# Optimization experiments

Hardware: AMD Instinct MI355X
Metric: run time of the kernel (lower is better)

## Reference

```python
import jax, jax.numpy as jnp
import numpy as np
from jax import lax

B, T, D = 8, 4096, 512
UNITS = 512
WINDOW = 2


def setup_inputs() -> dict:
    key = jax.random.key(0)
    k1, k2, k3 = jax.random.split(key, 3)
    x = jax.random.normal(k1, (B, T, D), dtype=jnp.float32)
    # keras kernel shape is (window, 1, input_dim, 3*units); drop the dummy height dim
    kernel = jax.random.uniform(k2, (WINDOW, D, 3 * UNITS), dtype=jnp.float32,
                                minval=-0.05, maxval=0.05)
    bias = jnp.zeros((3 * UNITS,), dtype=jnp.float32)
    return {"x": x, "kernel": kernel, "bias": bias}


def reference(x, kernel, bias):
    window, d_in, u3 = kernel.shape
    units = u3 // 3
    # causal padding: window-1 zeros on the left of the time axis
    xp = jnp.pad(x, ((0, 0), (window - 1, 0), (0, 0)))
    # 1D valid conv -> gates [B, T, 3*units]
    gates = lax.conv_general_dilated(
        xp, kernel, window_strides=(1,), padding='VALID',
        dimension_numbers=('NWC', 'WIO', 'NWC')) + bias
    z = jnp.tanh(gates[..., :units])
    f = jax.nn.sigmoid(gates[..., units:2 * units])
    o = jax.nn.sigmoid(gates[..., 2 * units:])

    # fo-pool recurrence: c_t = f_t * c_{t-1} + (1 - f_t) * z_t ; out_t = o_t * c_t
    def step(c, zfo):
        z_t, f_t, o_t = zfo
        c = f_t * c + (1.0 - f_t) * z_t
        return c, o_t * c

    c0 = jnp.zeros((x.shape[0], units), dtype=x.dtype)
    zT = jnp.swapaxes(z, 0, 1)  # [T, B, U]
    fT = jnp.swapaxes(f, 0, 1)
    oT = jnp.swapaxes(o, 0, 1)
    _, ysT = lax.scan(step, c0, (zT, fT, oT))
    return jnp.swapaxes(ysT, 0, 1)  # [B, T, U] (return_sequences=True)
```

## Files before the change

### kernel.cpp

```cpp
#include <hip/hip_runtime.h>
#include <cstdint>
#include <cstddef>

#define BB   8
#define TT   4096
#define DD   512
#define UU   512
#define NN   1536
#define KK   1024
#define MM   32768
#define NCH  256
#define CHL  16

using bf16x8 = __attribute__((ext_vector_type(8))) __bf16;
using f32x4  = __attribute__((ext_vector_type(4))) float;

__device__ __forceinline__ unsigned short f2bf(float f) {
    unsigned u = __float_as_uint(f);
    u += 0x7fffu + ((u >> 16) & 1u);
    return (unsigned short)(u >> 16);
}
__device__ __forceinline__ float bf2f(unsigned short s) {
    return __uint_as_float(((unsigned)s) << 16);
}
__device__ __forceinline__ float sigf(float x) { return 1.0f / (1.0f + __expf(-x)); }
__device__ __forceinline__ float tanh_(float x) { return 1.0f - 2.0f / (1.0f + __expf(2.0f * x)); }

__device__ __forceinline__ void async16(const void* g, void* l) {
    __builtin_amdgcn_global_load_lds(
        (__attribute__((address_space(1))) void*)g,
        (__attribute__((address_space(3))) void*)l, 16, 0, 0);
}

__global__ void k_prep(const float* __restrict__ x, unsigned short* __restrict__ xpad,
                       const float* __restrict__ kern, unsigned short* __restrict__ kT) {
    int bx = blockIdx.x;
    int by = blockIdx.y;
    int tid = threadIdx.x;
    if (bx < 2049) {
        int q = bx * 256 + tid;
        if (q >= 4097 * 128) return;
        int tp = q >> 7;
        int d  = (q & 127) << 2;
        size_t oi = ((size_t)by * 4097 + tp) * 512 + d;
        ushort4 o;
        if (tp == 0) {
            o.x = o.y = o.z = o.w = 0;
        } else {
            float4 v = *(const float4*)(x + ((size_t)by * 4096 + (tp - 1)) * 512 + d);
            o.x = f2bf(v.x); o.y = f2bf(v.y); o.z = f2bf(v.z); o.w = f2bf(v.w);
        }
        *(ushort4*)(xpad + oi) = o;
    } else {
        __shared__ float tile[32][33];
        int idx = (bx - 2049) * 8 + by;
        int c  = tid & 31;
        int r0 = tid >> 5;
        for (int t8 = 0; t8 < 8; ++t8) {
            int tnum = idx * 8 + t8;
            int k0 = (tnum & 31) * 32;
            int n0 = (tnum >> 5) * 32;
#pragma unroll
            for (int rr = r0; rr < 32; rr += 8)
                tile[rr][c] = kern[(size_t)(k0 + rr) * NN + n0 + c];
            __syncthreads();
#pragma unroll
            for (int rr = r0; rr < 32; rr += 8)
                kT[(size_t)(n0 + rr) * KK + k0 + c] = f2bf(tile[c][rr]);
            __syncthreads();
        }
    }
}


#define STAGE_A(BUF, KT, KH) do { \
    async16(xpad + abase + (size_t)rowS0 * 512 + ((KT) * 64 + (KH) * 32 + kcS0), \
            smem + (BUF) * 65536 + (KH) * 16384 + offL0); \
    async16(xpad + abase + (size_t)rowS1 * 512 + ((KT) * 64 + (KH) * 32 + kcS1), \
            smem + (BUF) * 65536 + (KH) * 16384 + offL1); \
} while (0)

#define STAGE_B(BUF, KT, KH) do { \
    async16(kTg + (size_t)(n0 + rowS0) * 1024 + ((KT) * 64 + (KH) * 32 + kcS0), \
            smem + (BUF) * 65536 + 32768 + (KH) * 16384 + offL0); \
    async16(kTg + (size_t)(n0 + rowS1) * 1024 + ((KT) * 64 + (KH) * 32 + kcS1), \
            smem + (BUF) * 65536 + 32768 + (KH) * 16384 + offL1); \
} while (0)

#define VM4 asm volatile("s_waitcnt vmcnt(4)" ::: "memory")
#define VM2 asm volatile("s_waitcnt vmcnt(2)" ::: "memory")
#define VM0 asm volatile("s_waitcnt vmcnt(0)" ::: "memory")

#define LDS_A(BUF, KS, MR) (*(const bf16x8*)(smem + (BUF) * 65536 + (KS) * 16384 + (MR) * 1024 + ldsA))
#define LDS_B(BUF, KS, NR) (*(const bf16x8*)(smem + (BUF) * 65536 + (KS) * 16384 + (NR) * 1024 + ldsB))

#define PH(DO_R, RBUF, RKS, RMH, AFN, LBN, BFN, AFC, BFC, MH, STG, VMW) \
    __builtin_amdgcn_s_barrier(); \
    if (DO_R) { \
        AFN[0] = LDS_A(RBUF, RKS, (RMH) * 4 + 0); \
        AFN[1] = LDS_A(RBUF, RKS, (RMH) * 4 + 1); \
        AFN[2] = LDS_A(RBUF, RKS, (RMH) * 4 + 2); \
        AFN[3] = LDS_A(RBUF, RKS, (RMH) * 4 + 3); \
        if (LBN) { \
            BFN[0] = LDS_B(RBUF, RKS, 0); \
            BFN[1] = LDS_B(RBUF, RKS, 1); \
            BFN[2] = LDS_B(RBUF, RKS, 2); \
            BFN[3] = LDS_B(RBUF, RKS, 3); \
        } \
    } \
    STG; \
    __builtin_amdgcn_sched_barrier(0); \
    __builtin_amdgcn_s_setprio(1); \
    acc[(MH)*4+0][0] = __builtin_amdgcn_mfma_f32_16x16x32_bf16(AFC[0], BFC[0], acc[(MH)*4+0][0], 0, 0, 0); \
    acc[(MH)*4+0][1] = __builtin_amdgcn_mfma_f32_16x16x32_bf16(AFC[0], BFC[1], acc[(MH)*4+0][1], 0, 0, 0); \
    acc[(MH)*4+0][2] = __builtin_amdgcn_mfma_f32_16x16x32_bf16(AFC[0], BFC[2], acc[(MH)*4+0][2], 0, 0, 0); \
    acc[(MH)*4+0][3] = __builtin_amdgcn_mfma_f32_16x16x32_bf16(AFC[0], BFC[3], acc[(MH)*4+0][3], 0, 0, 0); \
    acc[(MH)*4+1][0] = __builtin_amdgcn_mfma_f32_16x16x32_bf16(AFC[1], BFC[0], acc[(MH)*4+1][0], 0, 0, 0); \
    acc[(MH)*4+1][1] = __builtin_amdgcn_mfma_f32_16x16x32_bf16(AFC[1], BFC[1], acc[(MH)*4+1][1], 0, 0, 0); \
    acc[(MH)*4+1][2] = __builtin_amdgcn_mfma_f32_16x16x32_bf16(AFC[1], BFC[2], acc[(MH)*4+1][2], 0, 0, 0); \
    acc[(MH)*4+1][3] = __builtin_amdgcn_mfma_f32_16x16x32_bf16(AFC[1], BFC[3], acc[(MH)*4+1][3], 0, 0, 0); \
    acc[(MH)*4+2][0] = __builtin_amdgcn_mfma_f32_16x16x32_bf16(AFC[2], BFC[0], acc[(MH)*4+2][0], 0, 0, 0); \
    acc[(MH)*4+2][1] = __builtin_amdgcn_mfma_f32_16x16x32_bf16(AFC[2], BFC[1], acc[(MH)*4+2][1], 0, 0, 0); \
    acc[(MH)*4+2][2] = __builtin_amdgcn_mfma_f32_16x16x32_bf16(AFC[2], BFC[2], acc[(MH)*4+2][2], 0, 0, 0); \
    acc[(MH)*4+2][3] = __builtin_amdgcn_mfma_f32_16x16x32_bf16(AFC[2], BFC[3], acc[(MH)*4+2][3], 0, 0, 0); \
    acc[(MH)*4+3][0] = __builtin_amdgcn_mfma_f32_16x16x32_bf16(AFC[3], BFC[0], acc[(MH)*4+3][0], 0, 0, 0); \
    acc[(MH)*4+3][1] = __builtin_amdgcn_mfma_f32_16x16x32_bf16(AFC[3], BFC[1], acc[(MH)*4+3][1], 0, 0, 0); \
    acc[(MH)*4+3][2] = __builtin_amdgcn_mfma_f32_16x16x32_bf16(AFC[3], BFC[2], acc[(MH)*4+3][2], 0, 0, 0); \
    acc[(MH)*4+3][3] = __builtin_amdgcn_mfma_f32_16x16x32_bf16(AFC[3], BFC[3], acc[(MH)*4+3][3], 0, 0, 0); \
    __builtin_amdgcn_s_setprio(0); \
    VMW;

__global__ __launch_bounds__(512, 2) void k_gemm(
    const unsigned short* __restrict__ xpad,
    const unsigned short* __restrict__ kTg,
    const float* __restrict__ bias,
    unsigned short* __restrict__ gates)
{
    __shared__ char smem[131072];

    const int tid  = threadIdx.x;
    const int wid  = tid >> 6;
    const int lane = tid & 63;
    const int wr   = wid >> 2;
    const int wc   = wid & 3;
    const int lrow = lane & 15;
    const int quad = lane >> 4;

    const int bid = blockIdx.x;
    const int wg  = (bid & 7) * 96 + (bid >> 3);
    const int mt  = wg / 6;
    const int nt  = wg % 6;
    const int m0  = mt * 256;
    const int n0  = nt * 256;
    const int boff = m0 >> 12;
    const size_t abase = (size_t)(m0 + boff) * 512;

    const int off0 = (wid * 2 + 0) * 1024 + lane * 16;
    const int off1 = (wid * 2 + 1) * 1024 + lane * 16;
    const int ln0 = off0 >> 7, ln1 = off1 >> 7;
    const int g80 = ((off0 >> 4) & 7) ^ (ln0 & 7);
    const int g81 = ((off1 >> 4) & 7) ^ (ln1 & 7);
    const int offL0 = off0, offL1 = off1;
    const int rowS0 = ln0 * 2 + (g80 >> 2), rowS1 = ln1 * 2 + (g81 >> 2);
    const int kcS0 = (g80 & 3) * 8,         kcS1 = (g81 & 3) * 8;

    const int lh  = lrow >> 1;
    const int g8f = ((lrow & 1) * 4 + quad) ^ lh;
    const int ldsA = (wr * 64 + lh) * 128 + g8f * 16;
    const int ldsB = 32768 + (wc * 32 + lh) * 128 + g8f * 16;

    f32x4 acc[8][4] = {};
    bf16x8 afS0[4], afS1[4], bfS0[4], bfS1[4];

    STAGE_A(0, 0, 0); STAGE_B(0, 0, 0); STAGE_A(0, 0, 1); STAGE_B(0, 0, 1);
    VM4;
    __builtin_amdgcn_s_barrier();
    afS0[0] = LDS_A(0, 0, 0); afS0[1] = LDS_A(0, 0, 1);
    afS0[2] = LDS_A(0, 0, 2); afS0[3] = LDS_A(0, 0, 3);
    bfS0[0] = LDS_B(0, 0, 0); bfS0[1] = LDS_B(0, 0, 1);
    bfS0[2] = LDS_B(0, 0, 2); bfS0[3] = LDS_B(0, 0, 3);

    for (int i = 0; i < 7; ++i) {
        const int t1 = 2 * i + 1;
        const int t2 = 2 * i + 2;
        PH(1, 0, 0, 1, afS1, 0, bfS0, afS0, bfS0, 0, STAGE_A(1, t1, 0), VM2)
        PH(1, 0, 1, 0, afS0, 1, bfS1, afS1, bfS0, 1, STAGE_B(1, t1, 0), (void)0)
        PH(1, 0, 1, 1, afS1, 0, bfS0, afS0, bfS1, 0, STAGE_A(1, t1, 1), VM2)
        PH(1, 1, 0, 0, afS0, 1, bfS0, afS1, bfS1, 1, STAGE_B(1, t1, 1), (void)0)
        PH(1, 1, 0, 1, afS1, 0, bfS0, afS0, bfS0, 0, STAGE_A(0, t2, 0), VM2)
        PH(1, 1, 1, 0, afS0, 1, bfS1, afS1, bfS0, 1, STAGE_B(0, t2, 0), (void)0)
        PH(1, 1, 1, 1, afS1, 0, bfS0, afS0, bfS1, 0, STAGE_A(0, t2, 1), VM2)
        PH(1, 0, 0, 0, afS0, 1, bfS0, afS1, bfS1, 1, STAGE_B(0, t2, 1), (void)0)
    }
    {
        PH(1, 0, 0, 1, afS1, 0, bfS0, afS0, bfS0, 0, STAGE_A(1, 15, 0), VM2)
        PH(1, 0, 1, 0, afS0, 1, bfS1, afS1, bfS0, 1, STAGE_B(1, 15, 0), (void)0)
        PH(1, 0, 1, 1, afS1, 0, bfS0, afS0, bfS1, 0, STAGE_A(1, 15, 1), VM2)
        PH(1, 1, 0, 0, afS0, 1, bfS0, afS1, bfS1, 1, STAGE_B(1, 15, 1), (void)0)
        PH(1, 1, 0, 1, afS1, 0, bfS0, afS0, bfS0, 0, (void)0,           VM0)
        PH(1, 1, 1, 0, afS0, 1, bfS1, afS1, bfS0, 1, (void)0,           (void)0)
        PH(1, 1, 1, 1, afS1, 0, bfS0, afS0, bfS1, 0, (void)0,           (void)0)
        PH(0, 0, 0, 0, afS0, 0, bfS0, afS1, bfS1, 1, (void)0,           (void)0)
    }

    __syncthreads();
#pragma unroll
    for (int n = 0; n < 4; ++n) {
        int coll = wc * 64 + n * 16 + lrow;
        float bv = bias[n0 + coll];
        int g    = coll >> 3;
        int cb   = (coll & 7) * 2;
#pragma unroll
        for (int m = 0; m < 8; ++m) {
            int rbase = wr * 128 + m * 16 + quad * 4;
#pragma unroll
            for (int r = 0; r < 4; ++r) {
                int row = rbase + r;
                *(unsigned short*)(smem + row * 512 + ((g ^ (row & 7)) * 16) + cb)
                    = f2bf(acc[m][n][r] + bv);
            }
        }
    }
    __syncthreads();
    {
        unsigned short* gbase = gates + (size_t)m0 * NN + n0;
#pragma unroll
        for (int it = 0; it < 16; ++it) {
            int idx = it * 512 + tid;
            int row = idx >> 5;
            int g   = idx & 31;
            bf16x8 v = *(const bf16x8*)(smem + row * 512 + ((g ^ (row & 7)) * 16));
            *(bf16x8*)(gbase + (size_t)row * NN + g * 8) = v;
        }
    }
}

__global__ __launch_bounds__(128) void k_scanA(const unsigned short* __restrict__ gates,
                        float* __restrict__ Fp, float* __restrict__ Ce) {
    const int chunk = blockIdx.x;
    const int b     = blockIdx.y;
    const int u     = threadIdx.x << 2;
    const size_t g0 = ((size_t)b * TT + (size_t)chunk * CHL) * NN + u;

    float c0 = 0, c1 = 0, c2 = 0, c3 = 0;
    float F0 = 1, F1 = 1, F2 = 1, F3 = 1;

    ushort4 bz[8], bf_[8];
#pragma unroll
    for (int j = 0; j < 8; ++j) {
        bz[j]  = *(const ushort4*)(gates + g0 + (size_t)j * NN);
        bf_[j] = *(const ushort4*)(gates + g0 + (size_t)j * NN + UU);
    }
#pragma unroll
    for (int h = 0; h < 2; ++h) {
        ushort4 nz[8], nf[8];
        if (h == 0) {
#pragma unroll
            for (int j = 0; j < 8; ++j) {
                nz[j] = *(const ushort4*)(gates + g0 + (size_t)(8 + j) * NN);
                nf[j] = *(const ushort4*)(gates + g0 + (size_t)(8 + j) * NN + UU);
            }
        }
#pragma unroll
        for (int j = 0; j < 8; ++j) {
            float f0 = sigf(bf2f(bf_[j].x)), z0 = tanh_(bf2f(bz[j].x));
            float f1 = sigf(bf2f(bf_[j].y)), z1 = tanh_(bf2f(bz[j].y));
            float f2 = sigf(bf2f(bf_[j].z)), z2 = tanh_(bf2f(bz[j].z));
            float f3 = sigf(bf2f(bf_[j].w)), z3 = tanh_(bf2f(bz[j].w));
            c0 = f0 * c0 + (1.0f - f0) * z0; F0 *= f0;
            c1 = f1 * c1 + (1.0f - f1) * z1; F1 *= f1;
            c2 = f2 * c2 + (1.0f - f2) * z2; F2 *= f2;
            c3 = f3 * c3 + (1.0f - f3) * z3; F3 *= f3;
        }
        if (h == 0) {
#pragma unroll
            for (int j = 0; j < 8; ++j) { bz[j] = nz[j]; bf_[j] = nf[j]; }
        }
    }
    size_t ci = ((size_t)b * NCH + chunk) * UU + u;
    *(float4*)(Fp + ci) = make_float4(F0, F1, F2, F3);
    *(float4*)(Ce + ci) = make_float4(c0, c1, c2, c3);
}

__global__ __launch_bounds__(128) void k_scanB(const float* __restrict__ Fp,
                        const float* __restrict__ Ce, float* __restrict__ Cin) {
    int gid = blockIdx.x * 128 + threadIdx.x;
    int bb = gid >> 9;
    int uu = gid & 511;
    size_t base = (size_t)bb * NCH * UU + uu;
    float c = 0.0f;
    for (int k0 = 0; k0 < NCH; k0 += 8) {
        float F[8], E[8];
#pragma unroll
        for (int j = 0; j < 8; ++j) {
            F[j] = Fp[base + (size_t)(k0 + j) * UU];
            E[j] = Ce[base + (size_t)(k0 + j) * UU];
        }
#pragma unroll
        for (int j = 0; j < 8; ++j) {
            Cin[base + (size_t)(k0 + j) * UU] = c;
            c = F[j] * c + E[j];
        }
    }
}

__global__ __launch_bounds__(128) void k_scanC(const unsigned short* __restrict__ gates,
                        const float* __restrict__ Cin, float* __restrict__ out) {
    const int chunk = blockIdx.x;
    const int b     = blockIdx.y;
    const int u     = threadIdx.x << 2;
    const size_t g0 = ((size_t)b * TT + (size_t)chunk * CHL) * NN + u;
    size_t o = ((size_t)b * TT + (size_t)chunk * CHL) * UU + u;

    size_t ci = ((size_t)b * NCH + chunk) * UU + u;
    float4 cv = *(const float4*)(Cin + ci);
    float c0 = cv.x, c1 = cv.y, c2 = cv.z, c3 = cv.w;

    ushort4 bz[4], bf_[4], bo[4];
#pragma unroll
    for (int j = 0; j < 4; ++j) {
        bz[j]  = *(const ushort4*)(gates + g0 + (size_t)j * NN);
        bf_[j] = *(const ushort4*)(gates + g0 + (size_t)j * NN + UU);
        bo[j]  = *(const ushort4*)(gates + g0 + (size_t)j * NN + 2 * UU);
    }
#pragma unroll
    for (int k = 0; k < 4; ++k) {
        ushort4 nz[4], nf[4], no[4];
        if (k < 3) {
#pragma unroll
            for (int j = 0; j < 4; ++j) {
                size_t gg = g0 + (size_t)((k + 1) * 4 + j) * NN;
                nz[j] = *(const ushort4*)(gates + gg);
                nf[j] = *(const ushort4*)(gates + gg + UU);
                no[j] = *(const ushort4*)(gates + gg + 2 * UU);
            }
        }
#pragma unroll
        for (int j = 0; j < 4; ++j) {
            float f0 = sigf(bf2f(bf_[j].x)), z0 = tanh_(bf2f(bz[j].x)), o0 = sigf(bf2f(bo[j].x));
            float f1 = sigf(bf2f(bf_[j].y)), z1 = tanh_(bf2f(bz[j].y)), o1 = sigf(bf2f(bo[j].y));
            float f2 = sigf(bf2f(bf_[j].z)), z2 = tanh_(bf2f(bz[j].z)), o2 = sigf(bf2f(bo[j].z));
            float f3 = sigf(bf2f(bf_[j].w)), z3 = tanh_(bf2f(bz[j].w)), o3 = sigf(bf2f(bo[j].w));
            c0 = f0 * c0 + (1.0f - f0) * z0;
            c1 = f1 * c1 + (1.0f - f1) * z1;
            c2 = f2 * c2 + (1.0f - f2) * z2;
            c3 = f3 * c3 + (1.0f - f3) * z3;
            f32x4 ov = { o0 * c0, o1 * c1, o2 * c2, o3 * c3 };
            __builtin_nontemporal_store(ov, (f32x4*)(out + o));
            o += UU;
        }
        if (k < 3) {
#pragma unroll
            for (int j = 0; j < 4; ++j) { bz[j] = nz[j]; bf_[j] = nf[j]; bo[j] = no[j]; }
        }
    }
}

extern "C" void kernel_launch(void* const* d_in, const int* in_sizes, int n_in,
                              void* d_out, int out_size, void* d_ws, size_t ws_size,
                              hipStream_t stream) {
    const float* x    = (const float*)d_in[0];
    const float* kern = (const float*)d_in[1];
    const float* bias = (const float*)d_in[2];
    float* out = (float*)d_out;
    char* ws = (char*)d_ws;

    unsigned short* xpad  = (unsigned short*)(ws + 0);
    unsigned short* kT    = (unsigned short*)(ws + 33562624);
    unsigned short* gates = (unsigned short*)(ws + 36708352);
    float* Fp  = (float*)(ws + 137371648);
    float* Ce  = (float*)(ws + 141565952);
    float* Cin = (float*)(ws + 145760256);

    hipLaunchKernelGGL(k_prep,  dim3(2049 + 24, 8), dim3(256), 0, stream, x, xpad, kern, kT);
    hipLaunchKernelGGL(k_gemm,  dim3(768),          dim3(512), 0, stream, xpad, kT, bias, gates);
    hipLaunchKernelGGL(k_scanA, dim3(NCH, BB),      dim3(128), 0, stream, gates, Fp, Ce);
    hipLaunchKernelGGL(k_scanB, dim3(32),           dim3(128), 0, stream, Fp, Ce, Cin);
    hipLaunchKernelGGL(k_scanC, dim3(NCH, BB),      dim3(128), 0, stream, gates, Cin, out);
}
```

Measured before the change: 309.8 us.

## Fuse three-pass chunked scan into single decoupled-lookback scan kernel

```diff
diff --git a/kernel.cpp b/kernel.cpp
--- a/kernel.cpp
+++ b/kernel.cpp
@@ -9,8 +9,8 @@
 #define NN   1536
 #define KK   1024
 #define MM   32768
-#define NCH  256
-#define CHL  16
+#define NCH2 128
+#define CHL2 32
 
 using bf16x8 = __attribute__((ext_vector_type(8))) __bf16;
 using f32x4  = __attribute__((ext_vector_type(4))) float;
@@ -23,8 +23,12 @@
 __device__ __forceinline__ float bf2f(unsigned short s) {
     return __uint_as_float(((unsigned)s) << 16);
 }
-__device__ __forceinline__ float sigf(float x) { return 1.0f / (1.0f + __expf(-x)); }
-__device__ __forceinline__ float tanh_(float x) { return 1.0f - 2.0f / (1.0f + __expf(2.0f * x)); }
+__device__ __forceinline__ float sigf(float x) {
+    return __builtin_amdgcn_rcpf(1.0f + __expf(-x));
+}
+__device__ __forceinline__ float tanh_(float x) {
+    return 1.0f - 2.0f * __builtin_amdgcn_rcpf(1.0f + __expf(2.0f * x));
+}
 
 __device__ __forceinline__ void async16(const void* g, void* l) {
     __builtin_amdgcn_global_load_lds(
@@ -235,123 +239,162 @@
     }
 }
 
-__global__ __launch_bounds__(128) void k_scanA(const unsigned short* __restrict__ gates,
-                        float* __restrict__ Fp, float* __restrict__ Ce) {
-    const int chunk = blockIdx.x;
-    const int b     = blockIdx.y;
-    const int u     = threadIdx.x << 2;
-    const size_t g0 = ((size_t)b * TT + (size_t)chunk * CHL) * NN + u;
-
-    float c0 = 0, c1 = 0, c2 = 0, c3 = 0;
-    float F0 = 1, F1 = 1, F2 = 1, F3 = 1;
-
-    ushort4 bz[8], bf_[8];
-#pragma unroll
-    for (int j = 0; j < 8; ++j) {
-        bz[j]  = *(const ushort4*)(gates + g0 + (size_t)j * NN);
-        bf_[j] = *(const ushort4*)(gates + g0 + (size_t)j * NN + UU);
-    }
-#pragma unroll
-    for (int h = 0; h < 2; ++h) {
-        ushort4 nz[8], nf[8];
-        if (h == 0) {
-#pragma unroll
-            for (int j = 0; j < 8; ++j) {
-                nz[j] = *(const ushort4*)(gates + g0 + (size_t)(8 + j) * NN);
-                nf[j] = *(const ushort4*)(gates + g0 + (size_t)(8 + j) * NN + UU);
-            }
-        }
-#pragma unroll
-        for (int j = 0; j < 8; ++j) {
-            float f0 = sigf(bf2f(bf_[j].x)), z0 = tanh_(bf2f(bz[j].x));
-            float f1 = sigf(bf2f(bf_[j].y)), z1 = tanh_(bf2f(bz[j].y));
-            float f2 = sigf(bf2f(bf_[j].z)), z2 = tanh_(bf2f(bz[j].z));
-            float f3 = sigf(bf2f(bf_[j].w)), z3 = tanh_(bf2f(bz[j].w));
-            c0 = f0 * c0 + (1.0f - f0) * z0; F0 *= f0;
-            c1 = f1 * c1 + (1.0f - f1) * z1; F1 *= f1;
-            c2 = f2 * c2 + (1.0f - f2) * z2; F2 *= f2;
-            c3 = f3 * c3 + (1.0f - f3) * z3; F3 *= f3;
-        }
-        if (h == 0) {
-#pragma unroll
-            for (int j = 0; j < 8; ++j) { bz[j] = nz[j]; bf_[j] = nf[j]; }
-        }
-    }
-    size_t ci = ((size_t)b * NCH + chunk) * UU + u;
-    *(float4*)(Fp + ci) = make_float4(F0, F1, F2, F3);
-    *(float4*)(Ce + ci) = make_float4(c0, c1, c2, c3);
-}
-
-__global__ __launch_bounds__(128) void k_scanB(const float* __restrict__ Fp,
-                        const float* __restrict__ Ce, float* __restrict__ Cin) {
-    int gid = blockIdx.x * 128 + threadIdx.x;
-    int bb = gid >> 9;
-    int uu = gid & 511;
-    size_t base = (size_t)bb * NCH * UU + uu;
-    float c = 0.0f;
-    for (int k0 = 0; k0 < NCH; k0 += 8) {
-        float F[8], E[8];
-#pragma unroll
-        for (int j = 0; j < 8; ++j) {
-            F[j] = Fp[base + (size_t)(k0 + j) * UU];
-            E[j] = Ce[base + (size_t)(k0 + j) * UU];
-        }
-#pragma unroll
-        for (int j = 0; j < 8; ++j) {
-            Cin[base + (size_t)(k0 + j) * UU] = c;
-            c = F[j] * c + E[j];
-        }
-    }
-}
-
-__global__ __launch_bounds__(128) void k_scanC(const unsigned short* __restrict__ gates,
-                        const float* __restrict__ Cin, float* __restrict__ out) {
-    const int chunk = blockIdx.x;
-    const int b     = blockIdx.y;
-    const int u     = threadIdx.x << 2;
-    const size_t g0 = ((size_t)b * TT + (size_t)chunk * CHL) * NN + u;
-    size_t o = ((size_t)b * TT + (size_t)chunk * CHL) * UU + u;
-
-    size_t ci = ((size_t)b * NCH + chunk) * UU + u;
-    float4 cv = *(const float4*)(Cin + ci);
-    float c0 = cv.x, c1 = cv.y, c2 = cv.z, c3 = cv.w;
-
-    ushort4 bz[4], bf_[4], bo[4];
-#pragma unroll
-    for (int j = 0; j < 4; ++j) {
-        bz[j]  = *(const ushort4*)(gates + g0 + (size_t)j * NN);
-        bf_[j] = *(const ushort4*)(gates + g0 + (size_t)j * NN + UU);
-        bo[j]  = *(const ushort4*)(gates + g0 + (size_t)j * NN + 2 * UU);
-    }
-#pragma unroll
-    for (int k = 0; k < 4; ++k) {
-        ushort4 nz[4], nf[4], no[4];
-        if (k < 3) {
+__global__ __launch_bounds__(128, 4) void k_scan(
+    const unsigned short* __restrict__ gates,
+    float* AggF, float* AggE, float* Inc, unsigned* status,
+    float* __restrict__ out)
+{
+    const int bid   = blockIdx.x;
+    const int chunk = bid & (NCH2 - 1);
+    const int b     = bid >> 7;
+    const int tid   = threadIdx.x;
+    const int u     = tid << 2;
+    const size_t g0 = ((size_t)b * TT + (size_t)chunk * CHL2) * NN + u;
+    const size_t ai = ((size_t)b * NCH2 + chunk) * UU + u;
+    const int    si = b * NCH2 + chunk;
+
+    float c[4]  = {0.f, 0.f, 0.f, 0.f};
+    float Fa[4] = {1.f, 1.f, 1.f, 1.f};
+    {
+        ushort4 bz[4], bf4[4];
+#pragma unroll
+        for (int j = 0; j < 4; ++j) {
+            bz[j]  = *(const ushort4*)(gates + g0 + (size_t)j * NN);
+            bf4[j] = *(const ushort4*)(gates + g0 + (size_t)j * NN + UU);
+        }
+        for (int h = 0; h < 8; ++h) {
+            ushort4 nz[4], nf[4];
+            if (h < 7) {
+#pragma unroll
+                for (int j = 0; j < 4; ++j) {
+                    size_t gg = g0 + (size_t)((h + 1) * 4 + j) * NN;
+                    nz[j] = *(const ushort4*)(gates + gg);
+                    nf[j] = *(const ushort4*)(gates + gg + UU);
+                }
+            }
 #pragma unroll
             for (int j = 0; j < 4; ++j) {
-                size_t gg = g0 + (size_t)((k + 1) * 4 + j) * NN;
-                nz[j] = *(const ushort4*)(gates + gg);
-                nf[j] = *(const ushort4*)(gates + gg + UU);
-                no[j] = *(const ushort4*)(gates + gg + 2 * UU);
-            }
-        }
+                float f0 = sigf(bf2f(bf4[j].x)), z0 = tanh_(bf2f(bz[j].x));
+                float f1 = sigf(bf2f(bf4[j].y)), z1 = tanh_(bf2f(bz[j].y));
+                float f2 = sigf(bf2f(bf4[j].z)), z2 = tanh_(bf2f(bz[j].z));
+                float f3 = sigf(bf2f(bf4[j].w)), z3 = tanh_(bf2f(bz[j].w));
+                c[0] = f0 * c[0] + (1.0f - f0) * z0; Fa[0] *= f0;
+                c[1] = f1 * c[1] + (1.0f - f1) * z1; Fa[1] *= f1;
+                c[2] = f2 * c[2] + (1.0f - f2) * z2; Fa[2] *= f2;
+                c[3] = f3 * c[3] + (1.0f - f3) * z3; Fa[3] *= f3;
+            }
+            if (h < 7) {
+#pragma unroll
+                for (int j = 0; j < 4; ++j) { bz[j] = nz[j]; bf4[j] = nf[j]; }
+            }
+        }
+    }
+#pragma unroll
+    for (int e = 0; e < 4; ++e) {
+        __hip_atomic_store(AggF + ai + e, Fa[e], __ATOMIC_RELAXED, __HIP_MEMORY_SCOPE_AGENT);
+        __hip_atomic_store(AggE + ai + e, c[e],  __ATOMIC_RELAXED, __HIP_MEMORY_SCOPE_AGENT);
+    }
+    __threadfence();
+    __syncthreads();
+    if (tid == 0)
+        __hip_atomic_store(status + si, 1u, __ATOMIC_RELEASE, __HIP_MEMORY_SCOPE_AGENT);
+
+    float carry[4] = {0.f, 0.f, 0.f, 0.f};
+    if (chunk > 0) {
+        float runF[4] = {1.f, 1.f, 1.f, 1.f};
+        int k = chunk - 1;
+        for (;;) {
+            if (k < 0) break;
+            int nb = (k >= 3) ? 4 : (k + 1);
+            unsigned st[4];
+            float Fv[4][4], Ev[4][4], Iv[4][4];
+#pragma unroll
+            for (int j = 0; j < 4; ++j) {
+                if (j < nb)
+                    st[j] = __hip_atomic_load(status + b * NCH2 + (k - j),
+                                              __ATOMIC_ACQUIRE, __HIP_MEMORY_SCOPE_AGENT);
+            }
+#pragma unroll
+            for (int j = 0; j < 4; ++j) {
+                if (j < nb) {
+                    size_t aj = ((size_t)b * NCH2 + (k - j)) * UU + u;
+#pragma unroll
+                    for (int e = 0; e < 4; ++e) {
+                        Fv[j][e] = __hip_atomic_load(AggF + aj + e, __ATOMIC_RELAXED, __HIP_MEMORY_SCOPE_AGENT);
+                        Ev[j][e] = __hip_atomic_load(AggE + aj + e, __ATOMIC_RELAXED, __HIP_MEMORY_SCOPE_AGENT);
+                        Iv[j][e] = __hip_atomic_load(Inc  + aj + e, __ATOMIC_RELAXED, __HIP_MEMORY_SCOPE_AGENT);
+                    }
+                }
+            }
+            bool done = false;
+            int adv = nb;
+            for (int j = 0; j < nb; ++j) {
+                if (st[j] == 0u) { adv = j; break; }
+                if (st[j] == 2u) {
+#pragma unroll
+                    for (int e = 0; e < 4; ++e) carry[e] = fmaf(runF[e], Iv[j][e], carry[e]);
+                    done = true; break;
+                }
+#pragma unroll
+                for (int e = 0; e < 4; ++e) {
+                    carry[e] = fmaf(runF[e], Ev[j][e], carry[e]);
+                    runF[e] *= Fv[j][e];
+                }
+            }
+            if (done) break;
+            k -= adv;
+            if (adv == 0) __builtin_amdgcn_s_sleep(2);
+        }
+    }
+#pragma unroll
+    for (int e = 0; e < 4; ++e) {
+        float inc = fmaf(Fa[e], carry[e], c[e]);
+        __hip_atomic_store(Inc + ai + e, inc, __ATOMIC_RELAXED, __HIP_MEMORY_SCOPE_AGENT);
+    }
+    __threadfence();
+    __syncthreads();
+    if (tid == 0)
+        __hip_atomic_store(status + si, 2u, __ATOMIC_RELEASE, __HIP_MEMORY_SCOPE_AGENT);
+
+    {
+        float c0 = carry[0], c1 = carry[1], c2 = carry[2], c3 = carry[3];
+        size_t o = ((size_t)b * TT + (size_t)chunk * CHL2) * UU + u;
+        ushort4 bz[4], bf4[4], bo[4];
 #pragma unroll
         for (int j = 0; j < 4; ++j) {
-            float f0 = sigf(bf2f(bf_[j].x)), z0 = tanh_(bf2f(bz[j].x)), o0 = sigf(bf2f(bo[j].x));
-            float f1 = sigf(bf2f(bf_[j].y)), z1 = tanh_(bf2f(bz[j].y)), o1 = sigf(bf2f(bo[j].y));
-            float f2 = sigf(bf2f(bf_[j].z)), z2 = tanh_(bf2f(bz[j].z)), o2 = sigf(bf2f(bo[j].z));
-            float f3 = sigf(bf2f(bf_[j].w)), z3 = tanh_(bf2f(bz[j].w)), o3 = sigf(bf2f(bo[j].w));
-            c0 = f0 * c0 + (1.0f - f0) * z0;
-            c1 = f1 * c1 + (1.0f - f1) * z1;
-            c2 = f2 * c2 + (1.0f - f2) * z2;
-            c3 = f3 * c3 + (1.0f - f3) * z3;
-            f32x4 ov = { o0 * c0, o1 * c1, o2 * c2, o3 * c3 };
-            __builtin_nontemporal_store(ov, (f32x4*)(out + o));
-            o += UU;
-        }
-        if (k < 3) {
-#pragma unroll
-            for (int j = 0; j < 4; ++j) { bz[j] = nz[j]; bf_[j] = nf[j]; bo[j] = no[j]; }
+            bz[j]  = *(const ushort4*)(gates + g0 + (size_t)j * NN);
+            bf4[j] = *(const ushort4*)(gates + g0 + (size_t)j * NN + UU);
+            bo[j]  = *(const ushort4*)(gates + g0 + (size_t)j * NN + 2 * UU);
+        }
+        for (int h = 0; h < 8; ++h) {
+            ushort4 nz[4], nf[4], no[4];
+            if (h < 7) {
+#pragma unroll
+                for (int j = 0; j < 4; ++j) {
+                    size_t gg = g0 + (size_t)((h + 1) * 4 + j) * NN;
+                    nz[j] = *(const ushort4*)(gates + gg);
+                    nf[j] = *(const ushort4*)(gates + gg + UU);
+                    no[j] = *(const ushort4*)(gates + gg + 2 * UU);
+                }
+            }
+#pragma unroll
+            for (int j = 0; j < 4; ++j) {
+                float f0 = sigf(bf2f(bf4[j].x)), z0 = tanh_(bf2f(bz[j].x)), o0 = sigf(bf2f(bo[j].x));
+                float f1 = sigf(bf2f(bf4[j].y)), z1 = tanh_(bf2f(bz[j].y)), o1 = sigf(bf2f(bo[j].y));
+                float f2 = sigf(bf2f(bf4[j].z)), z2 = tanh_(bf2f(bz[j].z)), o2 = sigf(bf2f(bo[j].z));
+                float f3 = sigf(bf2f(bf4[j].w)), z3 = tanh_(bf2f(bz[j].w)), o3 = sigf(bf2f(bo[j].w));
+                c0 = f0 * c0 + (1.0f - f0) * z0;
+                c1 = f1 * c1 + (1.0f - f1) * z1;
+                c2 = f2 * c2 + (1.0f - f2) * z2;
+                c3 = f3 * c3 + (1.0f - f3) * z3;
+                f32x4 ov = { o0 * c0, o1 * c1, o2 * c2, o3 * c3 };
+                __builtin_nontemporal_store(ov, (f32x4*)(out + o));
+                o += UU;
+            }
+            if (h < 7) {
+#pragma unroll
+                for (int j = 0; j < 4; ++j) { bz[j] = nz[j]; bf4[j] = nf[j]; bo[j] = no[j]; }
+            }
         }
     }
 }
@@ -368,13 +411,14 @@
     unsigned short* xpad  = (unsigned short*)(ws + 0);
     unsigned short* kT    = (unsigned short*)(ws + 33562624);
     unsigned short* gates = (unsigned short*)(ws + 36708352);
-    float* Fp  = (float*)(ws + 137371648);
-    float* Ce  = (float*)(ws + 141565952);
-    float* Cin = (float*)(ws + 145760256);
+    float* AggF = (float*)(ws + 137371648);
+    float* AggE = (float*)(ws + 141565952);
+    float* Inc  = (float*)(ws + 145760256);
+    unsigned* status = (unsigned*)(ws + 33562624);
 
     hipLaunchKernelGGL(k_prep,  dim3(2049 + 24, 8), dim3(256), 0, stream, x, xpad, kern, kT);
     hipLaunchKernelGGL(k_gemm,  dim3(768),          dim3(512), 0, stream, xpad, kT, bias, gates);
-    hipLaunchKernelGGL(k_scanA, dim3(NCH, BB),      dim3(128), 0, stream, gates, Fp, Ce);
-    hipLaunchKernelGGL(k_scanB, dim3(32),           dim3(128), 0, stream, Fp, Ce, Cin);
-    hipLaunchKernelGGL(k_scanC, dim3(NCH, BB),      dim3(128), 0, stream, gates, Cin, out);
-}
+    hipMemsetAsync(status, 0, BB * NCH2 * sizeof(unsigned), stream);
+    hipLaunchKernelGGL(k_scan,  dim3(NCH2 * BB),    dim3(128), 0, stream,
+                       gates, AggF, AggE, Inc, status, out);
+}
```

Measured after the change: 817.3 us. 2.64x slower.

## Make GEMM persistent with three tiles per block and prefetch next tile

Applied to the files above, without the earlier changes.

```diff
diff --git a/kernel.cpp b/kernel.cpp
--- a/kernel.cpp
+++ b/kernel.cpp
@@ -73,17 +73,17 @@
 }
 
 
-#define STAGE_A(BUF, KT, KH) do { \
-    async16(xpad + abase + (size_t)rowS0 * 512 + ((KT) * 64 + (KH) * 32 + kcS0), \
+#define STAGE_A(ABASE, BUF, KT, KH) do { \
+    async16(xpad + (ABASE) + (size_t)rowS0 * 512 + ((KT) * 64 + (KH) * 32 + kcS0), \
             smem + (BUF) * 65536 + (KH) * 16384 + offL0); \
-    async16(xpad + abase + (size_t)rowS1 * 512 + ((KT) * 64 + (KH) * 32 + kcS1), \
+    async16(xpad + (ABASE) + (size_t)rowS1 * 512 + ((KT) * 64 + (KH) * 32 + kcS1), \
             smem + (BUF) * 65536 + (KH) * 16384 + offL1); \
 } while (0)
 
-#define STAGE_B(BUF, KT, KH) do { \
-    async16(kTg + (size_t)(n0 + rowS0) * 1024 + ((KT) * 64 + (KH) * 32 + kcS0), \
+#define STAGE_B(N0B, BUF, KT, KH) do { \
+    async16(kTg + (size_t)((N0B) + rowS0) * 1024 + ((KT) * 64 + (KH) * 32 + kcS0), \
             smem + (BUF) * 65536 + 32768 + (KH) * 16384 + offL0); \
-    async16(kTg + (size_t)(n0 + rowS1) * 1024 + ((KT) * 64 + (KH) * 32 + kcS1), \
+    async16(kTg + (size_t)((N0B) + rowS1) * 1024 + ((KT) * 64 + (KH) * 32 + kcS1), \
             smem + (BUF) * 65536 + 32768 + (KH) * 16384 + offL1); \
 } while (0)
 
@@ -147,13 +147,8 @@
     const int quad = lane >> 4;
 
     const int bid = blockIdx.x;
-    const int wg  = (bid & 7) * 96 + (bid >> 3);
-    const int mt  = wg / 6;
-    const int nt  = wg % 6;
-    const int m0  = mt * 256;
-    const int n0  = nt * 256;
-    const int boff = m0 >> 12;
-    const size_t abase = (size_t)(m0 + boff) * 512;
+    const int xcd = bid & 7;
+    const int sub = bid >> 3;
 
     const int off0 = (wid * 2 + 0) * 1024 + lane * 16;
     const int off1 = (wid * 2 + 1) * 1024 + lane * 16;
@@ -169,68 +164,95 @@
     const int ldsA = (wr * 64 + lh) * 128 + g8f * 16;
     const int ldsB = 32768 + (wc * 32 + lh) * 128 + g8f * 16;
 
-    f32x4 acc[8][4] = {};
-    bf16x8 afS0[4], afS1[4], bfS0[4], bfS1[4];
-
-    STAGE_A(0, 0, 0); STAGE_B(0, 0, 0); STAGE_A(0, 0, 1); STAGE_B(0, 0, 1);
-    VM4;
-    __builtin_amdgcn_s_barrier();
-    afS0[0] = LDS_A(0, 0, 0); afS0[1] = LDS_A(0, 0, 1);
-    afS0[2] = LDS_A(0, 0, 2); afS0[3] = LDS_A(0, 0, 3);
-    bfS0[0] = LDS_B(0, 0, 0); bfS0[1] = LDS_B(0, 0, 1);
-    bfS0[2] = LDS_B(0, 0, 2); bfS0[3] = LDS_B(0, 0, 3);
-
-    for (int i = 0; i < 7; ++i) {
-        const int t1 = 2 * i + 1;
-        const int t2 = 2 * i + 2;
-        PH(1, 0, 0, 1, afS1, 0, bfS0, afS0, bfS0, 0, STAGE_A(1, t1, 0), VM2)
-        PH(1, 0, 1, 0, afS0, 1, bfS1, afS1, bfS0, 1, STAGE_B(1, t1, 0), (void)0)
-        PH(1, 0, 1, 1, afS1, 0, bfS0, afS0, bfS1, 0, STAGE_A(1, t1, 1), VM2)
-        PH(1, 1, 0, 0, afS0, 1, bfS0, afS1, bfS1, 1, STAGE_B(1, t1, 1), (void)0)
-        PH(1, 1, 0, 1, afS1, 0, bfS0, afS0, bfS0, 0, STAGE_A(0, t2, 0), VM2)
-        PH(1, 1, 1, 0, afS0, 1, bfS1, afS1, bfS0, 1, STAGE_B(0, t2, 0), (void)0)
-        PH(1, 1, 1, 1, afS1, 0, bfS0, afS0, bfS1, 0, STAGE_A(0, t2, 1), VM2)
-        PH(1, 0, 0, 0, afS0, 1, bfS0, afS1, bfS1, 1, STAGE_B(0, t2, 1), (void)0)
-    }
-    {
-        PH(1, 0, 0, 1, afS1, 0, bfS0, afS0, bfS0, 0, STAGE_A(1, 15, 0), VM2)
-        PH(1, 0, 1, 0, afS0, 1, bfS1, afS1, bfS0, 1, STAGE_B(1, 15, 0), (void)0)
-        PH(1, 0, 1, 1, afS1, 0, bfS0, afS0, bfS1, 0, STAGE_A(1, 15, 1), VM2)
-        PH(1, 1, 0, 0, afS0, 1, bfS0, afS1, bfS1, 1, STAGE_B(1, 15, 1), (void)0)
-        PH(1, 1, 0, 1, afS1, 0, bfS0, afS0, bfS0, 0, (void)0,           VM0)
-        PH(1, 1, 1, 0, afS0, 1, bfS1, afS1, bfS0, 1, (void)0,           (void)0)
-        PH(1, 1, 1, 1, afS1, 0, bfS0, afS0, bfS1, 0, (void)0,           (void)0)
-        PH(0, 0, 0, 0, afS0, 0, bfS0, afS1, bfS1, 1, (void)0,           (void)0)
-    }
-
-    __syncthreads();
-#pragma unroll
-    for (int n = 0; n < 4; ++n) {
-        int coll = wc * 64 + n * 16 + lrow;
-        float bv = bias[n0 + coll];
-        int g    = coll >> 3;
-        int cb   = (coll & 7) * 2;
-#pragma unroll
-        for (int m = 0; m < 8; ++m) {
-            int rbase = wr * 128 + m * 16 + quad * 4;
-#pragma unroll
-            for (int r = 0; r < 4; ++r) {
-                int row = rbase + r;
-                *(unsigned short*)(smem + row * 512 + ((g ^ (row & 7)) * 16) + cb)
-                    = f2bf(acc[m][n][r] + bv);
+    for (int r = 0; r < 3; ++r) {
+        const int wgl = sub * 3 + r;
+        const int mt  = xcd * 16 + wgl / 6;
+        const int nt  = wgl % 6;
+        const int m0  = mt * 256;
+        const int n0  = nt * 256;
+        const int boff = m0 >> 12;
+        const size_t abase = (size_t)(m0 + boff) * 512;
+        const int wgl2 = wgl + 1;
+        const int mt2  = xcd * 16 + wgl2 / 6;
+        const int n0N  = (wgl2 % 6) * 256;
+        const int m02  = mt2 * 256;
+        const size_t abaseN = (size_t)(m02 + (m02 >> 12)) * 512;
+
+        f32x4 acc[8][4] = {};
+        bf16x8 afS0[4], afS1[4], bfS0[4], bfS1[4];
+
+        if (r == 0) {
+            STAGE_A(abase, 0, 0, 0); STAGE_B(n0, 0, 0, 0);
+            STAGE_A(abase, 0, 0, 1); STAGE_B(n0, 0, 0, 1);
+        }
+        VM4;
+        __builtin_amdgcn_s_barrier();
+        afS0[0] = LDS_A(0, 0, 0); afS0[1] = LDS_A(0, 0, 1);
+        afS0[2] = LDS_A(0, 0, 2); afS0[3] = LDS_A(0, 0, 3);
+        bfS0[0] = LDS_B(0, 0, 0); bfS0[1] = LDS_B(0, 0, 1);
+        bfS0[2] = LDS_B(0, 0, 2); bfS0[3] = LDS_B(0, 0, 3);
+
+        for (int i = 0; i < 7; ++i) {
+            const int t1 = 2 * i + 1;
+            const int t2 = 2 * i + 2;
+            PH(1, 0, 0, 1, afS1, 0, bfS0, afS0, bfS0, 0, STAGE_A(abase, 1, t1, 0), VM2)
+            PH(1, 0, 1, 0, afS0, 1, bfS1, afS1, bfS0, 1, STAGE_B(n0, 1, t1, 0), (void)0)
+            PH(1, 0, 1, 1, afS1, 0, bfS0, afS0, bfS1, 0, STAGE_A(abase, 1, t1, 1), VM2)
+            PH(1, 1, 0, 0, afS0, 1, bfS0, afS1, bfS1, 1, STAGE_B(n0, 1, t1, 1), (void)0)
+            PH(1, 1, 0, 1, afS1, 0, bfS0, afS0, bfS0, 0, STAGE_A(abase, 0, t2, 0), VM2)
+            PH(1, 1, 1, 0, afS0, 1, bfS1, afS1, bfS0, 1, STAGE_B(n0, 0, t2, 0), (void)0)
+            PH(1, 1, 1, 1, afS1, 0, bfS0, afS0, bfS1, 0, STAGE_A(abase, 0, t2, 1), VM2)
+            PH(1, 0, 0, 0, afS0, 1, bfS0, afS1, bfS1, 1, STAGE_B(n0, 0, t2, 1), (void)0)
+        }
+        {
+            PH(1, 0, 0, 1, afS1, 0, bfS0, afS0, bfS0, 0, STAGE_A(abase, 1, 15, 0), VM2)
+            PH(1, 0, 1, 0, afS0, 1, bfS1, afS1, bfS0, 1, STAGE_B(n0, 1, 15, 0), (void)0)
+            PH(1, 0, 1, 1, afS1, 0, bfS0, afS0, bfS1, 0, STAGE_A(abase, 1, 15, 1), VM2)
+            PH(1, 1, 0, 0, afS0, 1, bfS0, afS1, bfS1, 1, STAGE_B(n0, 1, 15, 1), (void)0)
+            PH(1, 1, 0, 1, afS1, 0, bfS0, afS0, bfS0, 0, if (r < 2) STAGE_A(abaseN, 0, 0, 0),
+               if (r < 2) { VM2; } else { VM0; })
+            PH(1, 1, 1, 0, afS0, 1, bfS1, afS1, bfS0, 1, if (r < 2) STAGE_B(n0N, 0, 0, 0), (void)0)
+            PH(1, 1, 1, 1, afS1, 0, bfS0, afS0, bfS1, 0, if (r < 2) STAGE_A(abaseN, 0, 0, 1), (void)0)
+            PH(0, 0, 0, 0, afS0, 0, bfS0, afS1, bfS1, 1, if (r < 2) STAGE_B(n0N, 0, 0, 1), (void)0)
+        }
+
+        __syncthreads();
+#pragma unroll
+        for (int half = 0; half < 2; ++half) {
+            if (wr == half) {
+#pragma unroll
+                for (int n = 0; n < 4; ++n) {
+                    int coll = wc * 64 + n * 16 + lrow;
+                    float bv = bias[n0 + coll];
+                    int g    = coll >> 3;
+                    int cb   = (coll & 7) * 2;
+#pragma unroll
+                    for (int m = 0; m < 8; ++m) {
+                        int lr0 = m * 16 + quad * 4;
+#pragma unroll
+                        for (int rr = 0; rr < 4; ++rr) {
+                            int row = lr0 + rr;
+                            *(unsigned short*)(smem + 65536 + row * 512 +
+                                               ((g ^ (row & 7)) * 16) + cb)
+                                = f2bf(acc[m][n][rr] + bv);
+                        }
+                    }
+                }
             }
-        }
-    }
-    __syncthreads();
-    {
-        unsigned short* gbase = gates + (size_t)m0 * NN + n0;
-#pragma unroll
-        for (int it = 0; it < 16; ++it) {
-            int idx = it * 512 + tid;
-            int row = idx >> 5;
-            int g   = idx & 31;
-            bf16x8 v = *(const bf16x8*)(smem + row * 512 + ((g ^ (row & 7)) * 16));
-            *(bf16x8*)(gbase + (size_t)row * NN + g * 8) = v;
+            __syncthreads();
+            {
+                unsigned short* gbase = gates + (size_t)(m0 + half * 128) * NN + n0;
+#pragma unroll
+                for (int it = 0; it < 8; ++it) {
+                    int idx = it * 512 + tid;
+                    int row = idx >> 5;
+                    int g   = idx & 31;
+                    bf16x8 v = *(const bf16x8*)(smem + 65536 + row * 512 +
+                                                ((g ^ (row & 7)) * 16));
+                    *(bf16x8*)(gbase + (size_t)row * NN + g * 8) = v;
+                }
+            }
+            __syncthreads();
         }
     }
 }
@@ -373,7 +395,7 @@
     float* Cin = (float*)(ws + 145760256);
 
     hipLaunchKernelGGL(k_prep,  dim3(2049 + 24, 8), dim3(256), 0, stream, x, xpad, kern, kT);
-    hipLaunchKernelGGL(k_gemm,  dim3(768),          dim3(512), 0, stream, xpad, kT, bias, gates);
+    hipLaunchKernelGGL(k_gemm,  dim3(256),          dim3(512), 0, stream, xpad, kT, bias, gates);
     hipLaunchKernelGGL(k_scanA, dim3(NCH, BB),      dim3(128), 0, stream, gates, Fp, Ce);
     hipLaunchKernelGGL(k_scanB, dim3(32),           dim3(128), 0, stream, Fp, Ce, Cin);
     hipLaunchKernelGGL(k_scanC, dim3(NCH, BB),      dim3(128), 0, stream, gates, Cin, out);
```

Result: slower. 490.7 us (+58.4%).
